# Performance work log

Measured on AMD Instinct MI355X. Metric: run time of the kernel, lower is better.

The kernel has to match this reference:

```python
import jax, jax.numpy as jnp
import numpy as np
import math

EMB_DIM = 1024
NUM_HEADS = 16
D_H = EMB_DIM // NUM_HEADS
B, S = 2, 2048


def setup_inputs() -> dict:
    key = jax.random.key(0)
    ks = jax.random.split(key, 6)
    limit = math.sqrt(6.0 / (EMB_DIM + D_H))  # xavier_uniform per head
    x = jax.random.normal(ks[0], (B, S, EMB_DIM), dtype=jnp.float32)
    Wq = jax.random.uniform(ks[1], (NUM_HEADS, EMB_DIM, D_H), jnp.float32, -limit, limit)
    Wk = jax.random.uniform(ks[2], (NUM_HEADS, EMB_DIM, D_H), jnp.float32, -limit, limit)
    Wv = jax.random.uniform(ks[3], (NUM_HEADS, EMB_DIM, D_H), jnp.float32, -limit, limit)
    bq = jnp.zeros((NUM_HEADS, D_H), jnp.float32)
    bk = jnp.zeros((NUM_HEADS, D_H), jnp.float32)
    bv = jnp.zeros((NUM_HEADS, D_H), jnp.float32)
    limo = math.sqrt(6.0 / (EMB_DIM + EMB_DIM))
    W_O = jax.random.uniform(ks[4], (EMB_DIM, EMB_DIM), jnp.float32, -limo, limo)
    causal_mask = jnp.tril(jnp.ones((S, S), jnp.float32))
    padding_mask = jnp.zeros((B, S), jnp.bool_)  # all-False: nothing padded
    return {"x": x, "Wq": Wq, "bq": bq, "Wk": Wk, "bk": bk, "Wv": Wv,
            "bv": bv, "W_O": W_O, "causal_mask": causal_mask,
            "padding_mask": padding_mask}


def reference(x, Wq, bq, Wk, bk, Wv, bv, W_O, causal_mask, padding_mask):
    # Per-head projections, vectorized over heads: [B,S,E] x [H,E,D] -> [B,H,S,D]
    Q = jnp.einsum('bse,hed->bhsd', x, Wq) + bq[None, :, None, :]
    K = jnp.einsum('bse,hed->bhsd', x, Wk) + bk[None, :, None, :]
    V = jnp.einsum('bse,hed->bhsd', x, Wv) + bv[None, :, None, :]
    scores = jnp.einsum('bhsd,bhtd->bhst', Q, K) / math.sqrt(D_H)
    neg_inf = jnp.float32(-jnp.inf)
    scores = jnp.where(causal_mask[None, None, :, :] == 0, neg_inf, scores)
    scores = jnp.where(padding_mask[:, None, None, :], neg_inf, scores)
    attn = jax.nn.softmax(scores, axis=-1)
    out = jnp.einsum('bhst,bhtd->bhsd', attn, V)  # [B,H,S,D]
    # concat heads in order (dim=-1) -> [B,S,H*D]
    x_concat = out.transpose(0, 2, 1, 3).reshape(B, S, EMB_DIM)
    return x_concat @ W_O
```

## Files before the change

### kernel.cpp

```cpp
#include <hip/hip_runtime.h>
#include <hip/hip_bf16.h>


typedef __hip_bfloat16 bf16;
typedef __attribute__((ext_vector_type(8))) short bfrag;
typedef __attribute__((ext_vector_type(4))) float f32x4;
typedef __attribute__((ext_vector_type(16))) float f32x16;
typedef __attribute__((ext_vector_type(4))) short short4v;

#define MFMA16(a, b, c) __builtin_amdgcn_mfma_f32_16x16x32_bf16(a, b, c, 0, 0, 0)
#define MFMA32(a, b, c) __builtin_amdgcn_mfma_f32_32x32x16_bf16(a, b, c, 0, 0, 0)

__global__ __launch_bounds__(256) void cast_f32_bf16(const float* __restrict__ src,
                                                     bf16* __restrict__ dst, int n) {
  int i = (blockIdx.x * 256 + threadIdx.x) * 8;
  if (i >= n) return;
  float4 a = *(const float4*)(src + i);
  float4 b = *(const float4*)(src + i + 4);
  union { bf16 h[8]; bfrag v; } tmp;
  tmp.h[0] = __float2bfloat16(a.x); tmp.h[1] = __float2bfloat16(a.y);
  tmp.h[2] = __float2bfloat16(a.z); tmp.h[3] = __float2bfloat16(a.w);
  tmp.h[4] = __float2bfloat16(b.x); tmp.h[5] = __float2bfloat16(b.y);
  tmp.h[6] = __float2bfloat16(b.z); tmp.h[7] = __float2bfloat16(b.w);
  *(bfrag*)(dst + i) = tmp.v;
}

__global__ __launch_bounds__(256) void prep_weights(const float* __restrict__ Wq,
                                                    const float* __restrict__ Wk,
                                                    const float* __restrict__ Wv,
                                                    const float* __restrict__ Wo,
                                                    bf16* __restrict__ WqkvT,
                                                    bf16* __restrict__ WoT) {
  __shared__ bf16 tile[64][80];
  int id = blockIdx.x;
  const float* src;
  bf16* dst;
  int srcld, dstld, r0, c0;
  if (id < 768) {
    int w = id >> 8, h = (id >> 4) & 15;
    r0 = (id & 15) * 64; c0 = 0;
    src = ((w == 0) ? Wq : (w == 1) ? Wk : Wv) + (long)h * 1024 * 64;
    dst = WqkvT + ((long)w * 1024 + h * 64) * 1024;
    srcld = 64; dstld = 1024;
  } else {
    int j = id - 768;
    c0 = (j & 15) * 64; r0 = (j >> 4) * 64;
    src = Wo; dst = WoT;
    srcld = 1024; dstld = 1024;
  }
  int t = threadIdx.x;
  int lr = t >> 3, lc = (t & 7) << 3;
#pragma unroll
  for (int p = 0; p < 2; ++p) {
    int r = lr + p * 32;
    const float* s = src + (long)(r0 + r) * srcld + c0 + lc;
    union { bf16 h8[8]; bfrag v; } tmp;
#pragma unroll
    for (int j = 0; j < 8; ++j) tmp.h8[j] = __float2bfloat16(s[j]);
    *(bfrag*)(&tile[r][lc]) = tmp.v;
  }
  __syncthreads();
#pragma unroll
  for (int p = 0; p < 2; ++p) {
    int c = lr + p * 32;
    union { bf16 h8[8]; bfrag v; } tmp;
#pragma unroll
    for (int j = 0; j < 8; ++j) tmp.h8[j] = tile[lc + j][c];
    *(bfrag*)(dst + (long)(c0 + c) * dstld + r0 + lc) = tmp.v;
  }
}

__global__ __launch_bounds__(256) void gemm_qkv128(const bf16* __restrict__ xb,
                                                   const bf16* __restrict__ WT,
                                                   const float* __restrict__ bq,
                                                   const float* __restrict__ bk,
                                                   const float* __restrict__ bv,
                                                   bf16* __restrict__ Q,
                                                   bf16* __restrict__ K_,
                                                   bf16* __restrict__ Vt) {
  const int K = 1024;
  __shared__ bf16 As[128][72];
  __shared__ bf16 Bs[128][72];
  int n0 = blockIdx.x * 128;
  int m0 = blockIdx.y * 128;
  int t = threadIdx.x, wave = t >> 6, lane = t & 63, quad = lane >> 4, col = lane & 15;
  int wr = (wave >> 1) * 64, wc = (wave & 1) * 64;
  f32x4 acc[4][4] = {};

  int srow = t >> 1, scol = (t & 1) * 32;
  const bf16* Ag = xb + (long)(m0 + srow) * K + scol;
  const bf16* Bg = WT + (long)(n0 + srow) * K + scol;

  bfrag Ar[4], Br[4];
#pragma unroll
  for (int i = 0; i < 4; ++i) {
    Ar[i] = *(const bfrag*)(Ag + 8 * i);
    Br[i] = *(const bfrag*)(Bg + 8 * i);
  }

  for (int k0 = 0; k0 < K; k0 += 64) {
    __syncthreads();
#pragma unroll
    for (int i = 0; i < 4; ++i) {
      *(bfrag*)(&As[srow][scol + 8 * i]) = Ar[i];
      *(bfrag*)(&Bs[srow][scol + 8 * i]) = Br[i];
    }
    int kn = (k0 + 64 < K) ? k0 + 64 : k0;
#pragma unroll
    for (int i = 0; i < 4; ++i) {
      Ar[i] = *(const bfrag*)(Ag + kn + 8 * i);
      Br[i] = *(const bfrag*)(Bg + kn + 8 * i);
    }
    __syncthreads();
#pragma unroll
    for (int kc = 0; kc < 2; ++kc) {
      bfrag ra[4], rb[4];
#pragma unroll
      for (int i = 0; i < 4; ++i)
        ra[i] = *(const bfrag*)(&As[wr + 16 * i + col][kc * 32 + quad * 8]);
#pragma unroll
      for (int c = 0; c < 4; ++c)
        rb[c] = *(const bfrag*)(&Bs[wc + 16 * c + col][kc * 32 + quad * 8]);
#pragma unroll
      for (int c = 0; c < 4; ++c)
#pragma unroll
        for (int i = 0; i < 4; ++i) acc[c][i] = MFMA16(ra[i], rb[c], acc[c][i]);
    }
  }

  int sel = n0 >> 10;
  const float* bias = (sel == 0) ? bq : (sel == 1) ? bk : bv;
#pragma unroll
  for (int c = 0; c < 4; ++c) {
    int n = n0 + wc + 16 * c + col;
    int nn = n & 1023;
    float bvv = bias[nn];
#pragma unroll
    for (int i = 0; i < 4; ++i) {
      int mb = m0 + wr + 16 * i + quad * 4;
      if (sel < 2) {
        bf16* dst = (sel == 0) ? Q : K_;
#pragma unroll
        for (int r = 0; r < 4; ++r)
          dst[(long)(mb + r) * 1024 + nn] = __float2bfloat16(acc[c][i][r] + bvv);
      } else {
        int b = mb >> 11, s0 = mb & 2047;
        int h = nn >> 6, d = nn & 63;
        union { bf16 h4[4]; short4v v; } pk;
#pragma unroll
        for (int r = 0; r < 4; ++r) pk.h4[r] = __float2bfloat16(acc[c][i][r] + bvv);
        *(short4v*)(Vt + (long)(((b << 4) + h) * 64 + d) * 2048 + s0) = pk.v;
      }
    }
  }
}

__global__ __launch_bounds__(256) void gemm_out(const bf16* __restrict__ A,
                                                const bf16* __restrict__ Bt,
                                                float* __restrict__ Cf) {
  const int K = 1024;
  __shared__ bf16 As[128][72];
  __shared__ bf16 Bs[64][72];
  int n0 = blockIdx.x * 64;
  int m0 = blockIdx.y * 128;
  int t = threadIdx.x;
  int wave = t >> 6, lane = t & 63, quad = lane >> 4, col = lane & 15;
  int wr = (wave >> 1) * 64, wc = (wave & 1) * 32;
  f32x4 acc[2][4] = {};

  int srA = t >> 1, scA = (t & 1) * 32;
  int srB = t >> 2, scB = (t & 3) * 16;
  const bf16* Ag = A + (long)(m0 + srA) * K + scA;
  const bf16* Bg = Bt + (long)(n0 + srB) * K + scB;

  bfrag Ar[4], Br[2];
#pragma unroll
  for (int i = 0; i < 4; ++i) Ar[i] = *(const bfrag*)(Ag + 8 * i);
#pragma unroll
  for (int i = 0; i < 2; ++i) Br[i] = *(const bfrag*)(Bg + 8 * i);

  for (int k0 = 0; k0 < K; k0 += 64) {
    __syncthreads();
#pragma unroll
    for (int i = 0; i < 4; ++i) *(bfrag*)(&As[srA][scA + 8 * i]) = Ar[i];
#pragma unroll
    for (int i = 0; i < 2; ++i) *(bfrag*)(&Bs[srB][scB + 8 * i]) = Br[i];
    int kn = (k0 + 64 < K) ? k0 + 64 : k0;
#pragma unroll
    for (int i = 0; i < 4; ++i) Ar[i] = *(const bfrag*)(Ag + kn + 8 * i);
#pragma unroll
    for (int i = 0; i < 2; ++i) Br[i] = *(const bfrag*)(Bg + kn + 8 * i);
    __syncthreads();
#pragma unroll
    for (int kc = 0; kc < 2; ++kc) {
      bfrag ra[4], rb[2];
#pragma unroll
      for (int i = 0; i < 4; ++i)
        ra[i] = *(const bfrag*)(&As[wr + 16 * i + col][kc * 32 + quad * 8]);
#pragma unroll
      for (int c = 0; c < 2; ++c)
        rb[c] = *(const bfrag*)(&Bs[wc + 16 * c + col][kc * 32 + quad * 8]);
#pragma unroll
      for (int c = 0; c < 2; ++c)
#pragma unroll
        for (int i = 0; i < 4; ++i) acc[c][i] = MFMA16(ra[i], rb[c], acc[c][i]);
    }
  }

#pragma unroll
  for (int c = 0; c < 2; ++c) {
    int n = n0 + wc + 16 * c + col;
#pragma unroll
    for (int i = 0; i < 4; ++i)
#pragma unroll
      for (int r = 0; r < 4; ++r) {
        int m = m0 + wr + 16 * i + quad * 4 + r;
        Cf[(long)m * 1024 + n] = acc[c][i][r];
      }
  }
}

__global__ __launch_bounds__(256) void attn_kernel(const bf16* __restrict__ Qc,
                                                   const bf16* __restrict__ Kc,
                                                   const bf16* __restrict__ Vt,
                                                   bf16* __restrict__ O) {
  int pair = blockIdx.x;
  int bh = blockIdx.y;
  int b = bh >> 4, h = bh & 15;

  __shared__ bf16 Ks[128][72];
  __shared__ bf16 Vs[64][136];
  __shared__ bf16 Ps[64][136];

  int t = threadIdx.x, wave = t >> 6, lane = t & 63;
  int qh = wave >> 1, jh = wave & 1, hi = lane >> 5, l5 = lane & 31;

  const float SC2 = 0.18033688f;

  int krow = t >> 3, kg = (t & 7) * 8;
  int vrow = t >> 4, vg = (t & 15) * 8;
  const bf16* Kbase = Kc + (long)(b * 2048 + krow) * 1024 + h * 64 + kg;
  const bf16* Vbase = Vt + (long)(bh * 64 + vrow) * 2048 + vg;

#pragma unroll
  for (int qsel = 0; qsel < 2; ++qsel) {
    int qt = qsel ? (31 - pair) : pair;
    int q0 = qt * 64;
    int nj = (qt >> 1) + 1;

    bfrag qa[4];
    const bf16* qp = Qc + (long)(b * 2048 + q0 + 32 * qh + l5) * 1024 + h * 64 + hi * 8;
#pragma unroll
    for (int kd = 0; kd < 4; ++kd) qa[kd] = *(const bfrag*)(qp + kd * 16);

    f32x16 o0, o1;
    float lsum[16];
#pragma unroll
    for (int r = 0; r < 16; ++r) { o0[r] = 0.f; o1[r] = 0.f; lsum[r] = 0.f; }

    bfrag kreg[4], vreg[4];
#pragma unroll
    for (int i = 0; i < 4; ++i)
      kreg[i] = *(const bfrag*)(Kbase + (long)(32 * i) * 1024);

    for (int jt = 0; jt < nj; ++jt) {
      int j0 = jt * 128;
      __syncthreads();
#pragma unroll
      for (int i = 0; i < 4; ++i)
        *(bfrag*)(&Ks[krow + 32 * i][kg]) = kreg[i];
      int jn = (jt + 1 < nj) ? (jt + 1) * 128 : jt * 128;
#pragma unroll
      for (int i = 0; i < 4; ++i)
        vreg[i] = *(const bfrag*)(Vbase + (long)(16 * i) * 2048 + j0);
#pragma unroll
      for (int i = 0; i < 4; ++i)
        kreg[i] = *(const bfrag*)(Kbase + (long)(jn + 32 * i) * 1024);
      __syncthreads();

      f32x16 s0, s1;
#pragma unroll
      for (int r = 0; r < 16; ++r) { s0[r] = 0.f; s1[r] = 0.f; }
#pragma unroll
      for (int kd = 0; kd < 4; ++kd) {
        bfrag kb0 = *(const bfrag*)(&Ks[jh * 64 + l5][kd * 16 + hi * 8]);
        bfrag kb1 = *(const bfrag*)(&Ks[jh * 64 + 32 + l5][kd * 16 + hi * 8]);
        s0 = MFMA32(qa[kd], kb0, s0);
        s1 = MFMA32(qa[kd], kb1, s1);
      }

      bool lastT = (jt == nj - 1);
#pragma unroll
      for (int jb = 0; jb < 2; ++jb) {
        int j = j0 + jh * 64 + jb * 32 + l5;
#pragma unroll
        for (int r = 0; r < 16; ++r) {
          int qrow = (r & 3) + 8 * (r >> 2) + 4 * hi;
          float sv = jb ? s1[r] : s0[r];
          float p = __builtin_amdgcn_exp2f(fmaf(sv, SC2, -16.0f));
          if (lastT) p = (j <= q0 + 32 * qh + qrow) ? p : 0.f;
          lsum[r] += p;
          Ps[32 * qh + qrow][jh * 64 + jb * 32 + l5] = __float2bfloat16(p);
        }
      }
#pragma unroll
      for (int i = 0; i < 4; ++i)
        *(bfrag*)(&Vs[vrow + 16 * i][vg]) = vreg[i];
      __syncthreads();

#pragma unroll
      for (int kj = 0; kj < 4; ++kj) {
        bfrag pa = *(const bfrag*)(&Ps[32 * qh + l5][jh * 64 + kj * 16 + hi * 8]);
        bfrag vb0 = *(const bfrag*)(&Vs[l5][jh * 64 + kj * 16 + hi * 8]);
        bfrag vb1 = *(const bfrag*)(&Vs[32 + l5][jh * 64 + kj * 16 + hi * 8]);
        o0 = MFMA32(pa, vb0, o0);
        o1 = MFMA32(pa, vb1, o1);
      }
    }

#pragma unroll
    for (int off = 1; off < 32; off <<= 1)
#pragma unroll
      for (int r = 0; r < 16; ++r) lsum[r] += __shfl_xor(lsum[r], off, 64);

    __syncthreads();
    float* Osc = (float*)&Ps[0][0];
    float* Lsc = (float*)&Vs[0][0];
    if (jh == 1) {
#pragma unroll
      for (int r = 0; r < 16; ++r) {
        int qrow = (r & 3) + 8 * (r >> 2) + 4 * hi;
        Osc[(qh * 32 + qrow) * 68 + 0 * 32 + l5] = o0[r];
        Osc[(qh * 32 + qrow) * 68 + 1 * 32 + l5] = o1[r];
      }
      if (l5 == 0) {
#pragma unroll
        for (int r = 0; r < 16; ++r) {
          int qrow = (r & 3) + 8 * (r >> 2) + 4 * hi;
          Lsc[qh * 32 + qrow] = lsum[r];
        }
      }
    }
    __syncthreads();
    if (jh == 0) {
#pragma unroll
      for (int r = 0; r < 16; ++r) {
        int qrow = (r & 3) + 8 * (r >> 2) + 4 * hi;
        float inv = 1.f / (lsum[r] + Lsc[qh * 32 + qrow]);
        int iq = q0 + 32 * qh + qrow;
        float v0 = o0[r] + Osc[(qh * 32 + qrow) * 68 + 0 * 32 + l5];
        float v1 = o1[r] + Osc[(qh * 32 + qrow) * 68 + 1 * 32 + l5];
        O[(long)(b * 2048 + iq) * 1024 + h * 64 + l5] = __float2bfloat16(v0 * inv);
        O[(long)(b * 2048 + iq) * 1024 + h * 64 + 32 + l5] = __float2bfloat16(v1 * inv);
      }
    }
  }
}

extern "C" void kernel_launch(void* const* d_in, const int* in_sizes, int n_in,
                              void* d_out, int out_size, void* d_ws, size_t ws_size,
                              hipStream_t stream) {
  const float* x  = (const float*)d_in[0];
  const float* Wq = (const float*)d_in[1];
  const float* bq = (const float*)d_in[2];
  const float* Wk = (const float*)d_in[3];
  const float* bk = (const float*)d_in[4];
  const float* Wv = (const float*)d_in[5];
  const float* bv = (const float*)d_in[6];
  const float* Wo = (const float*)d_in[7];
  float* out = (float*)d_out;

  bf16* ws = (bf16*)d_ws;
  const long MB1 = 1 << 20;
  bf16* WqkvT = ws + 0 * MB1;
  bf16* WoT   = ws + 3 * MB1;
  bf16* Q     = ws + 4 * MB1;
  bf16* K_    = ws + 8 * MB1;
  bf16* Vt    = ws + 12 * MB1;
  bf16* O     = ws + 16 * MB1;
  bf16* xb    = ws + 20 * MB1;

  cast_f32_bf16<<<2048, 256, 0, stream>>>(x, xb, 4096 * 1024);
  prep_weights<<<1024, 256, 0, stream>>>(Wq, Wk, Wv, Wo, WqkvT, WoT);

  gemm_qkv128<<<dim3(24, 32), 256, 0, stream>>>(xb, WqkvT, bq, bk, bv, Q, K_, Vt);

  attn_kernel<<<dim3(16, 32), 256, 0, stream>>>(Q, K_, Vt, O);

  gemm_out<<<dim3(16, 32), 256, 0, stream>>>(O, WoT, out);
}
```

Baseline: 212.2 us.

## Fuse prep kernels, head-major Q/K/O layout, XCD-aware block mapping, deeper prefetch

The input cast and weight transposes are merged into one kernel launch. Q, K and O are now stored head-major ([b,h,s,d]), so the attention loads become contiguous 128-byte rows instead of strided 2KB rows. Block indices in all three main kernels are remapped so that blocks sharing operands land on the same XCD for L2 reuse. The GEMMs also prefetch two K-steps ahead in registers, which raises register pressure, and the output GEMM now reads O with a strided head-major pattern.

```diff
diff --git a/kernel.cpp b/kernel.cpp
--- a/kernel.cpp
+++ b/kernel.cpp
@@ -11,44 +11,45 @@
 #define MFMA16(a, b, c) __builtin_amdgcn_mfma_f32_16x16x32_bf16(a, b, c, 0, 0, 0)
 #define MFMA32(a, b, c) __builtin_amdgcn_mfma_f32_32x32x16_bf16(a, b, c, 0, 0, 0)
 
-__global__ __launch_bounds__(256) void cast_f32_bf16(const float* __restrict__ src,
-                                                     bf16* __restrict__ dst, int n) {
-  int i = (blockIdx.x * 256 + threadIdx.x) * 8;
-  if (i >= n) return;
-  float4 a = *(const float4*)(src + i);
-  float4 b = *(const float4*)(src + i + 4);
-  union { bf16 h[8]; bfrag v; } tmp;
-  tmp.h[0] = __float2bfloat16(a.x); tmp.h[1] = __float2bfloat16(a.y);
-  tmp.h[2] = __float2bfloat16(a.z); tmp.h[3] = __float2bfloat16(a.w);
-  tmp.h[4] = __float2bfloat16(b.x); tmp.h[5] = __float2bfloat16(b.y);
-  tmp.h[6] = __float2bfloat16(b.z); tmp.h[7] = __float2bfloat16(b.w);
-  *(bfrag*)(dst + i) = tmp.v;
-}
-
-__global__ __launch_bounds__(256) void prep_weights(const float* __restrict__ Wq,
-                                                    const float* __restrict__ Wk,
-                                                    const float* __restrict__ Wv,
-                                                    const float* __restrict__ Wo,
-                                                    bf16* __restrict__ WqkvT,
-                                                    bf16* __restrict__ WoT) {
+__global__ __launch_bounds__(256) void prep_all(const float* __restrict__ x,
+                                                const float* __restrict__ Wq,
+                                                const float* __restrict__ Wk,
+                                                const float* __restrict__ Wv,
+                                                const float* __restrict__ Wo,
+                                                bf16* __restrict__ xb,
+                                                bf16* __restrict__ WqkvT,
+                                                bf16* __restrict__ WoT) {
   __shared__ bf16 tile[64][80];
   int id = blockIdx.x;
+  int t = threadIdx.x;
+  if (id < 2048) {
+    int i = id * 2048 + t * 8;
+    float4 a = *(const float4*)(x + i);
+    float4 b = *(const float4*)(x + i + 4);
+    union { bf16 h[8]; bfrag v; } tmp;
+    tmp.h[0] = __float2bfloat16(a.x); tmp.h[1] = __float2bfloat16(a.y);
+    tmp.h[2] = __float2bfloat16(a.z); tmp.h[3] = __float2bfloat16(a.w);
+    tmp.h[4] = __float2bfloat16(b.x); tmp.h[5] = __float2bfloat16(b.y);
+    tmp.h[6] = __float2bfloat16(b.z); tmp.h[7] = __float2bfloat16(b.w);
+    *(bfrag*)(xb + i) = tmp.v;
+    return;
+  }
+  int wid = id - 2048;
   const float* src;
   bf16* dst;
   int srcld, dstld, r0, c0;
-  if (id < 768) {
-    int w = id >> 8, h = (id >> 4) & 15;
-    r0 = (id & 15) * 64; c0 = 0;
+  if (wid < 768) {
+    int w = wid >> 8, h = (wid >> 4) & 15;
+    r0 = (wid & 15) * 64; c0 = 0;
     src = ((w == 0) ? Wq : (w == 1) ? Wk : Wv) + (long)h * 1024 * 64;
     dst = WqkvT + ((long)w * 1024 + h * 64) * 1024;
     srcld = 64; dstld = 1024;
   } else {
-    int j = id - 768;
+    int j = wid - 768;
     c0 = (j & 15) * 64; r0 = (j >> 4) * 64;
     src = Wo; dst = WoT;
     srcld = 1024; dstld = 1024;
   }
-  int t = threadIdx.x;
   int lr = t >> 3, lc = (t & 7) << 3;
 #pragma unroll
   for (int p = 0; p < 2; ++p) {
@@ -81,8 +82,10 @@
   const int K = 1024;
   __shared__ bf16 As[128][72];
   __shared__ bf16 Bs[128][72];
-  int n0 = blockIdx.x * 128;
-  int m0 = blockIdx.y * 128;
+  int id = blockIdx.x;
+  int xcd = id & 7, s = id >> 3;
+  int m0 = ((xcd << 2) | (s & 3)) * 128;
+  int n0 = (s >> 2) * 128;
   int t = threadIdx.x, wave = t >> 6, lane = t & 63, quad = lane >> 4, col = lane & 15;
   int wr = (wave >> 1) * 64, wc = (wave & 1) * 64;
   f32x4 acc[4][4] = {};
@@ -91,25 +94,28 @@
   const bf16* Ag = xb + (long)(m0 + srow) * K + scol;
   const bf16* Bg = WT + (long)(n0 + srow) * K + scol;
 
-  bfrag Ar[4], Br[4];
+  bfrag A0[4], B0[4], A1[4], B1[4];
 #pragma unroll
   for (int i = 0; i < 4; ++i) {
-    Ar[i] = *(const bfrag*)(Ag + 8 * i);
-    Br[i] = *(const bfrag*)(Bg + 8 * i);
+    A0[i] = *(const bfrag*)(Ag + 8 * i);
+    B0[i] = *(const bfrag*)(Bg + 8 * i);
+    A1[i] = *(const bfrag*)(Ag + 64 + 8 * i);
+    B1[i] = *(const bfrag*)(Bg + 64 + 8 * i);
   }
 
   for (int k0 = 0; k0 < K; k0 += 64) {
     __syncthreads();
 #pragma unroll
     for (int i = 0; i < 4; ++i) {
-      *(bfrag*)(&As[srow][scol + 8 * i]) = Ar[i];
-      *(bfrag*)(&Bs[srow][scol + 8 * i]) = Br[i];
-    }
-    int kn = (k0 + 64 < K) ? k0 + 64 : k0;
+      *(bfrag*)(&As[srow][scol + 8 * i]) = A0[i];
+      *(bfrag*)(&Bs[srow][scol + 8 * i]) = B0[i];
+    }
+    int kn = (k0 + 128 < K) ? k0 + 128 : K - 64;
 #pragma unroll
     for (int i = 0; i < 4; ++i) {
-      Ar[i] = *(const bfrag*)(Ag + kn + 8 * i);
-      Br[i] = *(const bfrag*)(Bg + kn + 8 * i);
+      A0[i] = A1[i]; B0[i] = B1[i];
+      A1[i] = *(const bfrag*)(Ag + kn + 8 * i);
+      B1[i] = *(const bfrag*)(Bg + kn + 8 * i);
     }
     __syncthreads();
 #pragma unroll
@@ -132,20 +138,20 @@
   const float* bias = (sel == 0) ? bq : (sel == 1) ? bk : bv;
 #pragma unroll
   for (int c = 0; c < 4; ++c) {
-    int n = n0 + wc + 16 * c + col;
-    int nn = n & 1023;
+    int nn = (n0 + wc + 16 * c + col) & 1023;
     float bvv = bias[nn];
+    int h = nn >> 6, d = nn & 63;
 #pragma unroll
     for (int i = 0; i < 4; ++i) {
       int mb = m0 + wr + 16 * i + quad * 4;
+      int b = mb >> 11, s0 = mb & 2047;
       if (sel < 2) {
         bf16* dst = (sel == 0) ? Q : K_;
+        long base = ((long)((b << 4) + h) * 2048 + s0) * 64 + d;
 #pragma unroll
         for (int r = 0; r < 4; ++r)
-          dst[(long)(mb + r) * 1024 + nn] = __float2bfloat16(acc[c][i][r] + bvv);
+          dst[base + (long)r * 64] = __float2bfloat16(acc[c][i][r] + bvv);
       } else {
-        int b = mb >> 11, s0 = mb & 2047;
-        int h = nn >> 6, d = nn & 63;
         union { bf16 h4[4]; short4v v; } pk;
 #pragma unroll
         for (int r = 0; r < 4; ++r) pk.h4[r] = __float2bfloat16(acc[c][i][r] + bvv);
@@ -155,14 +161,16 @@
   }
 }
 
-__global__ __launch_bounds__(256) void gemm_out(const bf16* __restrict__ A,
+__global__ __launch_bounds__(256) void gemm_out(const bf16* __restrict__ O,
                                                 const bf16* __restrict__ Bt,
                                                 float* __restrict__ Cf) {
   const int K = 1024;
   __shared__ bf16 As[128][72];
   __shared__ bf16 Bs[64][72];
-  int n0 = blockIdx.x * 64;
-  int m0 = blockIdx.y * 128;
+  int id = blockIdx.x;
+  int xcd = id & 7, s = id >> 3;
+  int m0 = ((xcd << 2) | (s & 3)) * 128;
+  int n0 = (s >> 2) * 64;
   int t = threadIdx.x;
   int wave = t >> 6, lane = t & 63, quad = lane >> 4, col = lane & 15;
   int wr = (wave >> 1) * 64, wc = (wave & 1) * 32;
@@ -170,26 +178,41 @@
 
   int srA = t >> 1, scA = (t & 1) * 32;
   int srB = t >> 2, scB = (t & 3) * 16;
-  const bf16* Ag = A + (long)(m0 + srA) * K + scA;
+  int mrow = m0 + srA;
+  int ob = mrow >> 11, os = mrow & 2047;
+  const bf16* Ag = O + (long)ob * 2097152 + (long)os * 64 + scA;
   const bf16* Bg = Bt + (long)(n0 + srB) * K + scB;
 
-  bfrag Ar[4], Br[2];
-#pragma unroll
-  for (int i = 0; i < 4; ++i) Ar[i] = *(const bfrag*)(Ag + 8 * i);
-#pragma unroll
-  for (int i = 0; i < 2; ++i) Br[i] = *(const bfrag*)(Bg + 8 * i);
+  bfrag A0[4], A1[4];
+  bfrag B0[2], B1[2];
+#pragma unroll
+  for (int i = 0; i < 4; ++i) {
+    A0[i] = *(const bfrag*)(Ag + 8 * i);
+    A1[i] = *(const bfrag*)(Ag + (long)64 * 2048 + 8 * i);
+  }
+#pragma unroll
+  for (int i = 0; i < 2; ++i) {
+    B0[i] = *(const bfrag*)(Bg + 8 * i);
+    B1[i] = *(const bfrag*)(Bg + 64 + 8 * i);
+  }
 
   for (int k0 = 0; k0 < K; k0 += 64) {
     __syncthreads();
 #pragma unroll
-    for (int i = 0; i < 4; ++i) *(bfrag*)(&As[srA][scA + 8 * i]) = Ar[i];
-#pragma unroll
-    for (int i = 0; i < 2; ++i) *(bfrag*)(&Bs[srB][scB + 8 * i]) = Br[i];
-    int kn = (k0 + 64 < K) ? k0 + 64 : k0;
-#pragma unroll
-    for (int i = 0; i < 4; ++i) Ar[i] = *(const bfrag*)(Ag + kn + 8 * i);
-#pragma unroll
-    for (int i = 0; i < 2; ++i) Br[i] = *(const bfrag*)(Bg + kn + 8 * i);
+    for (int i = 0; i < 4; ++i) *(bfrag*)(&As[srA][scA + 8 * i]) = A0[i];
+#pragma unroll
+    for (int i = 0; i < 2; ++i) *(bfrag*)(&Bs[srB][scB + 8 * i]) = B0[i];
+    int kn = (k0 + 128 < K) ? k0 + 128 : K - 64;
+#pragma unroll
+    for (int i = 0; i < 4; ++i) {
+      A0[i] = A1[i];
+      A1[i] = *(const bfrag*)(Ag + (long)kn * 2048 + 8 * i);
+    }
+#pragma unroll
+    for (int i = 0; i < 2; ++i) {
+      B0[i] = B1[i];
+      B1[i] = *(const bfrag*)(Bg + kn + 8 * i);
+    }
     __syncthreads();
 #pragma unroll
     for (int kc = 0; kc < 2; ++kc) {
@@ -220,13 +243,14 @@
   }
 }
 
-__global__ __launch_bounds__(256) void attn_kernel(const bf16* __restrict__ Qc,
-                                                   const bf16* __restrict__ Kc,
+__global__ __launch_bounds__(256) void attn_kernel(const bf16* __restrict__ Q,
+                                                   const bf16* __restrict__ K_,
                                                    const bf16* __restrict__ Vt,
                                                    bf16* __restrict__ O) {
-  int pair = blockIdx.x;
-  int bh = blockIdx.y;
-  int b = bh >> 4, h = bh & 15;
+  int id = blockIdx.x;
+  int xcd = id & 7, kk = id >> 3;
+  int bh = ((kk & 3) << 3) | xcd;
+  int pair = kk >> 2;
 
   __shared__ bf16 Ks[128][72];
   __shared__ bf16 Vs[64][136];
@@ -239,8 +263,8 @@
 
   int krow = t >> 3, kg = (t & 7) * 8;
   int vrow = t >> 4, vg = (t & 15) * 8;
-  const bf16* Kbase = Kc + (long)(b * 2048 + krow) * 1024 + h * 64 + kg;
-  const bf16* Vbase = Vt + (long)(bh * 64 + vrow) * 2048 + vg;
+  const bf16* Kbase = K_ + ((long)bh * 2048 + krow) * 64 + kg;
+  const bf16* Vbase = Vt + ((long)bh * 64 + vrow) * 2048 + vg;
 
 #pragma unroll
   for (int qsel = 0; qsel < 2; ++qsel) {
@@ -249,7 +273,7 @@
     int nj = (qt >> 1) + 1;
 
     bfrag qa[4];
-    const bf16* qp = Qc + (long)(b * 2048 + q0 + 32 * qh + l5) * 1024 + h * 64 + hi * 8;
+    const bf16* qp = Q + ((long)bh * 2048 + q0 + 32 * qh + l5) * 64 + hi * 8;
 #pragma unroll
     for (int kd = 0; kd < 4; ++kd) qa[kd] = *(const bfrag*)(qp + kd * 16);
 
@@ -261,7 +285,7 @@
     bfrag kreg[4], vreg[4];
 #pragma unroll
     for (int i = 0; i < 4; ++i)
-      kreg[i] = *(const bfrag*)(Kbase + (long)(32 * i) * 1024);
+      kreg[i] = *(const bfrag*)(Kbase + (long)(32 * i) * 64);
 
     for (int jt = 0; jt < nj; ++jt) {
       int j0 = jt * 128;
@@ -275,7 +299,7 @@
         vreg[i] = *(const bfrag*)(Vbase + (long)(16 * i) * 2048 + j0);
 #pragma unroll
       for (int i = 0; i < 4; ++i)
-        kreg[i] = *(const bfrag*)(Kbase + (long)(jn + 32 * i) * 1024);
+        kreg[i] = *(const bfrag*)(Kbase + (long)(jn + 32 * i) * 64);
       __syncthreads();
 
       f32x16 s0, s1;
@@ -350,8 +374,8 @@
         int iq = q0 + 32 * qh + qrow;
         float v0 = o0[r] + Osc[(qh * 32 + qrow) * 68 + 0 * 32 + l5];
         float v1 = o1[r] + Osc[(qh * 32 + qrow) * 68 + 1 * 32 + l5];
-        O[(long)(b * 2048 + iq) * 1024 + h * 64 + l5] = __float2bfloat16(v0 * inv);
-        O[(long)(b * 2048 + iq) * 1024 + h * 64 + 32 + l5] = __float2bfloat16(v1 * inv);
+        O[((long)bh * 2048 + iq) * 64 + l5] = __float2bfloat16(v0 * inv);
+        O[((long)bh * 2048 + iq) * 64 + 32 + l5] = __float2bfloat16(v1 * inv);
       }
     }
   }
@@ -380,12 +404,8 @@
   bf16* O     = ws + 16 * MB1;
   bf16* xb    = ws + 20 * MB1;
 
-  cast_f32_bf16<<<2048, 256, 0, stream>>>(x, xb, 4096 * 1024);
-  prep_weights<<<1024, 256, 0, stream>>>(Wq, Wk, Wv, Wo, WqkvT, WoT);
-
-  gemm_qkv128<<<dim3(24, 32), 256, 0, stream>>>(xb, WqkvT, bq, bk, bv, Q, K_, Vt);
-
-  attn_kernel<<<dim3(16, 32), 256, 0, stream>>>(Q, K_, Vt, O);
-
-  gemm_out<<<dim3(16, 32), 256, 0, stream>>>(O, WoT, out);
+  prep_all<<<3072, 256, 0, stream>>>(x, Wq, Wk, Wv, Wo, xb, WqkvT, WoT);
+  gemm_qkv128<<<768, 256, 0, stream>>>(xb, WqkvT, bq, bk, bv, Q, K_, Vt);
+  attn_kernel<<<512, 256, 0, stream>>>(Q, K_, Vt, O);
+  gemm_out<<<512, 256, 0, stream>>>(O, WoT, out);
 }
```

New measurement: 211.2 us. No clear change (-0.5%).
